# Kernel optimization log

Hardware: AMD Instinct MI355X
Metric: run time of the kernel (lower is better)

Reference implementation:

```python
import jax, jax.numpy as jnp
import numpy as np

N, E = 50000, 800000          # nodes, edges
IN, H, C = 256, 4, 64          # in_channels, heads, per-head out channels
HID, OUT = 64, 40              # lin1 hidden, num classes
NEG_SLOPE = 0.2                # PyG GATConv default


def setup_inputs() -> dict:
    key = jax.random.key(0)
    ks = jax.random.split(key, 10)
    s = 0.05
    return {
        "x": jax.random.normal(ks[0], (N, IN), jnp.float32),
        "edge_index": jax.random.randint(ks[1], (2, E), 0, N, dtype=jnp.int64),
        "W": jax.random.normal(ks[2], (IN, H * C), jnp.float32) * s,     # GATConv lin (no bias)
        "att_src": jax.random.normal(ks[3], (H, C), jnp.float32) * s,
        "att_dst": jax.random.normal(ks[4], (H, C), jnp.float32) * s,
        "bias_conv": jnp.zeros((H * C,), jnp.float32),
        "W1": jax.random.normal(ks[5], (H * C, HID), jnp.float32) * s,
        "b1": jnp.zeros((HID,), jnp.float32),
        "W2": jax.random.normal(ks[6], (HID, OUT), jnp.float32) * s,
        "b2": jnp.zeros((OUT,), jnp.float32),
    }


def reference(x, edge_index, W, att_src, att_dst, bias_conv, W1, b1, W2, b2):
    n = x.shape[0]
    # PyG GATConv default: add self-loops (also guarantees no empty segments)
    loop = jnp.arange(n, dtype=edge_index.dtype)
    src = jnp.concatenate([edge_index[0], loop])  # [E+N]
    dst = jnp.concatenate([edge_index[1], loop])

    h = (x @ W).reshape(n, H, C)                         # [N,H,C]
    a_src = jnp.einsum('nhc,hc->nh', h, att_src)         # [N,H]
    a_dst = jnp.einsum('nhc,hc->nh', h, att_dst)

    # per-edge attention logits + segment softmax over incoming edges of dst
    e = jax.nn.leaky_relu(a_src[src] + a_dst[dst], NEG_SLOPE)   # [E+N,H]
    m = jax.ops.segment_max(e, dst, num_segments=n)             # [N,H]
    ex = jnp.exp(e - m[dst])
    denom = jax.ops.segment_sum(ex, dst, num_segments=n)
    alpha = ex / denom[dst]                                     # [E+N,H]

    # weighted scatter-aggregate of source features
    msg = alpha[:, :, None] * h[src]                            # [E+N,H,C]
    out = jax.ops.segment_sum(msg, dst, num_segments=n)         # [N,H,C]
    out = out.reshape(n, H * C) + bias_conv

    out = jax.nn.relu(out)              # .relu() after conv1 (dropout off in eval)
    out = jax.nn.relu(out @ W1 + b1)    # lin1 + relu
    return out @ W2 + b2                # lin2
```

## Files before the change

### kernel.cpp

```cpp
#include <hip/hip_runtime.h>
#include <math.h>

#define HEADS 4
#define CH 64
#define HC 256
#define SLOPE 0.2f
#define SLOT 64

typedef __attribute__((ext_vector_type(8))) short bf16x8;
typedef __attribute__((ext_vector_type(8))) unsigned short u16x8;
typedef __attribute__((ext_vector_type(4))) float f32x4;

__device__ __forceinline__ float4 ld4(const float* p){ return *(const float4*)p; }
__device__ __forceinline__ void st4(float* p, float4 v){ *(float4*)p = v; }
__device__ __forceinline__ float lrelu(float x){ return x > 0.f ? x : SLOPE * x; }
__device__ __forceinline__ unsigned short f2bf(float f){
  union { float f; unsigned int u; } v; v.f = f;
  unsigned int r = v.u + 0x7fffu + ((v.u >> 16) & 1u);
  return (unsigned short)(r >> 16);
}
__device__ __forceinline__ float bflo(unsigned int u){
  union { unsigned int u; float f; } v; v.u = u << 16; return v.f;
}
__device__ __forceinline__ float bfhi(unsigned int u){
  union { unsigned int u; float f; } v; v.u = u & 0xffff0000u; return v.f;
}
__device__ __forceinline__ void split2(float v, unsigned short& h, unsigned short& l){
  unsigned int u = __float_as_uint(v);
  h = (unsigned short)(u >> 16);
  float hf = __uint_as_float(u & 0xffff0000u);
  l = (unsigned short)(__float_as_uint(v - hf) >> 16);
}
__device__ __forceinline__ void dma16(const unsigned short* g, unsigned short* l){
  __builtin_amdgcn_global_load_lds(
      (const __attribute__((address_space(1))) unsigned int*)g,
      (__attribute__((address_space(3))) unsigned int*)l, 16, 0, 0);
}

__global__ __launch_bounds__(256) void k_pre(
    const float* __restrict__ W, const float* __restrict__ W1, const float* __restrict__ W2,
    unsigned short* __restrict__ Bhi, unsigned short* __restrict__ Blo,
    unsigned short* __restrict__ W1h, unsigned short* __restrict__ W1l,
    unsigned short* __restrict__ W2h, unsigned short* __restrict__ W2l,
    int* __restrict__ cnt, int Nn) {
  int b = blockIdx.x, t = threadIdx.x;
  if (b < 256) {
    int nn = b;
    unsigned short h, l;
    split2(W[(size_t)t*256 + nn], h, l);
    Bhi[(size_t)nn*256 + t] = h; Blo[(size_t)nn*256 + t] = l;
  } else if (b < 320) {
    int nn = b - 256;
    unsigned short h, l;
    split2(W1[(size_t)t*64 + nn], h, l);
    W1h[(size_t)nn*256 + t] = h; W1l[(size_t)nn*256 + t] = l;
  } else if (b < 368) {
    if (t < 64) {
      int nn = b - 320;
      float v = (nn < 40) ? W2[(size_t)t*40 + nn] : 0.f;
      unsigned short h, l;
      split2(v, h, l);
      W2h[(size_t)nn*64 + t] = h; W2l[(size_t)nn*64 + t] = l;
    }
  } else {
    int i = (b - 368)*256 + t;
    if (i < Nn) cnt[i] = 0;
  }
}

__global__ __launch_bounds__(256, 4) void k_gemmfill(const float* __restrict__ x,
    const unsigned short* __restrict__ Bhi_t, const unsigned short* __restrict__ Blo_t,
    unsigned short* __restrict__ hbf,
    const float* __restrict__ att_src, const float* __restrict__ att_dst,
    float* __restrict__ a_srcO, float* __restrict__ a_dstO, int M, int nFill,
    const int* __restrict__ ei, int* __restrict__ cnt, int* __restrict__ csrf,
    int E, int EN) {
  __shared__ __align__(16) unsigned short L[4*4096];
  int t = threadIdx.x;
  int b = blockIdx.x;
  if (b < nFill) {
    int base = b*2048 + t;
    int s0=0,d0=0,s1=0,d1=0,s2=0,d2=0,s3=0,d3=0;
    int s4=0,d4=0,s5=0,d5=0,s6=0,d6=0,s7=0,d7=0;
    int e0=base, e1=base+256, e2=base+512, e3=base+768;
    int e4=base+1024, e5=base+1280, e6=base+1536, e7=base+1792;
    bool q0=e0<EN,q1=e1<EN,q2=e2<EN,q3=e3<EN,q4=e4<EN,q5=e5<EN,q6=e6<EN,q7=e7<EN;
    if (q0) { if (e0<E) { s0=ei[e0]; d0=ei[E+e0]; } else { s0=e0-E; d0=s0; } }
    if (q1) { if (e1<E) { s1=ei[e1]; d1=ei[E+e1]; } else { s1=e1-E; d1=s1; } }
    if (q2) { if (e2<E) { s2=ei[e2]; d2=ei[E+e2]; } else { s2=e2-E; d2=s2; } }
    if (q3) { if (e3<E) { s3=ei[e3]; d3=ei[E+e3]; } else { s3=e3-E; d3=s3; } }
    if (q4) { if (e4<E) { s4=ei[e4]; d4=ei[E+e4]; } else { s4=e4-E; d4=s4; } }
    if (q5) { if (e5<E) { s5=ei[e5]; d5=ei[E+e5]; } else { s5=e5-E; d5=s5; } }
    if (q6) { if (e6<E) { s6=ei[e6]; d6=ei[E+e6]; } else { s6=e6-E; d6=s6; } }
    if (q7) { if (e7<E) { s7=ei[e7]; d7=ei[E+e7]; } else { s7=e7-E; d7=s7; } }
    if (q0) { int p = atomicAdd(&cnt[d0], 1); csrf[(d0<<6) + p] = s0; }
    if (q1) { int p = atomicAdd(&cnt[d1], 1); csrf[(d1<<6) + p] = s1; }
    if (q2) { int p = atomicAdd(&cnt[d2], 1); csrf[(d2<<6) + p] = s2; }
    if (q3) { int p = atomicAdd(&cnt[d3], 1); csrf[(d3<<6) + p] = s3; }
    if (q4) { int p = atomicAdd(&cnt[d4], 1); csrf[(d4<<6) + p] = s4; }
    if (q5) { int p = atomicAdd(&cnt[d5], 1); csrf[(d5<<6) + p] = s5; }
    if (q6) { int p = atomicAdd(&cnt[d6], 1); csrf[(d6<<6) + p] = s6; }
    if (q7) { int p = atomicAdd(&cnt[d7], 1); csrf[(d7<<6) + p] = s7; }
    return;
  }
  int gb = b - nFill;
  int lane = t & 63, w = t >> 6;
  int wr = w >> 1, wc = w & 1;
  int ln15 = lane & 15, lq = lane >> 4;
  int row0 = (gb >> 1) * 128, col0 = (gb & 1) * 128;

  f32x4 acc[4][4];
  #pragma unroll
  for (int i=0;i<4;i++)
    #pragma unroll
    for (int j=0;j<4;j++) acc[i][j] = (f32x4){0.f,0.f,0.f,0.f};

  int sA = w*128 + lane;
  int sB = sA + 64;
  int RA = sA>>3, uA = (sA&7)^(RA&7), idxA = (RA<<1)|(uA&1), segA = uA>>1;
  int RB = sB>>3, uB = (sB&7)^(RB&7), idxB = (RB<<1)|(uB&1), segB = uB>>1;
  size_t gB_a = (size_t)(col0+idxA)*256 + segA*8;
  size_t gB_b = (size_t)(col0+idxB)*256 + segB*8;
  int l0 = (w*128)*8, l1 = (w*128+64)*8;

  int ar = t >> 1, akh = t & 1;
  int arow = row0 + ar;
  bool avalid = arow < M;
  const float* xp = &x[(size_t)arow*256 + akh*16];
  int aR = ar >> 1;
  int u0w = ((2*akh+0) << 1) | (ar & 1);
  int u1w = ((2*akh+1) << 1) | (ar & 1);
  int as0 = aR*8 + (u0w ^ (aR & 7));
  int as1 = aR*8 + (u1w ^ (aR & 7));

  for (int c = 0; c < 8; c++) {
    int k0 = c*32;
    dma16(Bhi_t + gB_a + k0, &L[2*4096 + l0]);
    dma16(Bhi_t + gB_b + k0, &L[2*4096 + l1]);
    dma16(Blo_t + gB_a + k0, &L[3*4096 + l0]);
    dma16(Blo_t + gB_b + k0, &L[3*4096 + l1]);
    float4 f0 = make_float4(0,0,0,0), f1 = f0, f2 = f0, f3 = f0;
    if (avalid) {
      const float* xc = xp + k0;
      f0 = ld4(xc); f1 = ld4(xc+4); f2 = ld4(xc+8); f3 = ld4(xc+12);
    }
    u16x8 h0, l0v, h1, l1v;
    unsigned short hh, ll;
    split2(f0.x,hh,ll); h0[0]=hh; l0v[0]=ll;
    split2(f0.y,hh,ll); h0[1]=hh; l0v[1]=ll;
    split2(f0.z,hh,ll); h0[2]=hh; l0v[2]=ll;
    split2(f0.w,hh,ll); h0[3]=hh; l0v[3]=ll;
    split2(f1.x,hh,ll); h0[4]=hh; l0v[4]=ll;
    split2(f1.y,hh,ll); h0[5]=hh; l0v[5]=ll;
    split2(f1.z,hh,ll); h0[6]=hh; l0v[6]=ll;
    split2(f1.w,hh,ll); h0[7]=hh; l0v[7]=ll;
    split2(f2.x,hh,ll); h1[0]=hh; l1v[0]=ll;
    split2(f2.y,hh,ll); h1[1]=hh; l1v[1]=ll;
    split2(f2.z,hh,ll); h1[2]=hh; l1v[2]=ll;
    split2(f2.w,hh,ll); h1[3]=hh; l1v[3]=ll;
    split2(f3.x,hh,ll); h1[4]=hh; l1v[4]=ll;
    split2(f3.y,hh,ll); h1[5]=hh; l1v[5]=ll;
    split2(f3.z,hh,ll); h1[6]=hh; l1v[6]=ll;
    split2(f3.w,hh,ll); h1[7]=hh; l1v[7]=ll;
    *(u16x8*)&L[0*4096 + as0*8] = h0;
    *(u16x8*)&L[1*4096 + as0*8] = l0v;
    *(u16x8*)&L[0*4096 + as1*8] = h1;
    *(u16x8*)&L[1*4096 + as1*8] = l1v;
    __syncthreads();

    bf16x8 bh[4], bl[4];
    #pragma unroll
    for (int j = 0; j < 4; j++) {
      int nn = wc*64 + j*16 + ln15;
      int R = nn >> 1, u = (lq << 1) | (nn & 1);
      int s = R*8 + (u ^ (R & 7));
      bh[j] = *(bf16x8*)&L[2*4096 + s*8];
      bl[j] = *(bf16x8*)&L[3*4096 + s*8];
    }
    #pragma unroll
    for (int i = 0; i < 4; i++) {
      int r = wr*64 + i*16 + ln15;
      int R = r >> 1, u = (lq << 1) | (r & 1);
      int s = R*8 + (u ^ (R & 7));
      bf16x8 ah = *(bf16x8*)&L[0*4096 + s*8];
      bf16x8 al = *(bf16x8*)&L[1*4096 + s*8];
      #pragma unroll
      for (int j = 0; j < 4; j++) {
        acc[i][j] = __builtin_amdgcn_mfma_f32_16x16x32_bf16(ah, bh[j], acc[i][j], 0,0,0);
        acc[i][j] = __builtin_amdgcn_mfma_f32_16x16x32_bf16(al, bh[j], acc[i][j], 0,0,0);
        acc[i][j] = __builtin_amdgcn_mfma_f32_16x16x32_bf16(ah, bl[j], acc[i][j], 0,0,0);
      }
    }
    __syncthreads();
  }
  unsigned short* hb2 = hbf + (size_t)(gb & 1) * M * 128;
  #pragma unroll
  for (int i = 0; i < 4; i++) {
    #pragma unroll
    for (int r = 0; r < 4; r++) {
      int row = row0 + wr*64 + i*16 + lq*4 + r;
      if (row < M) {
        #pragma unroll
        for (int j = 0; j < 4; j++) {
          int col = wc*64 + j*16 + ln15;
          hb2[(size_t)row*128 + col] = f2bf(acc[i][j][r]);
        }
      }
    }
  }
  int head = (gb & 1)*2 + wc;
  float asv[4], adv[4];
  #pragma unroll
  for (int j=0;j<4;j++){
    asv[j] = att_src[head*CH + j*16 + ln15];
    adv[j] = att_dst[head*CH + j*16 + ln15];
  }
  #pragma unroll
  for (int i = 0; i < 4; i++) {
    #pragma unroll
    for (int r = 0; r < 4; r++) {
      float ps = acc[i][0][r]*asv[0] + acc[i][1][r]*asv[1]
               + acc[i][2][r]*asv[2] + acc[i][3][r]*asv[3];
      float pd = acc[i][0][r]*adv[0] + acc[i][1][r]*adv[1]
               + acc[i][2][r]*adv[2] + acc[i][3][r]*adv[3];
      #pragma unroll
      for (int m=8; m>=1; m>>=1) { ps += __shfl_xor(ps, m); pd += __shfl_xor(pd, m); }
      if (ln15 == 0) {
        int row = row0 + wr*64 + i*16 + lq*4 + r;
        if (row < M) { a_srcO[row*4+head] = ps; a_dstO[row*4+head] = pd; }
      }
    }
  }
}

__global__ __launch_bounds__(256) void k_gat(const unsigned short* __restrict__ hbf,
    const float* __restrict__ a_src, const float* __restrict__ a_dst,
    const int* __restrict__ cnt, const int* __restrict__ csrf,
    const float* __restrict__ bias, unsigned short* __restrict__ outbf,
    int N, int nBlk) {
  int w = threadIdx.x >> 6, lane = threadIdx.x & 63;
  int q = lane >> 4, cl = lane & 15;
  int pass = (blockIdx.x >= nBlk) ? 1 : 0;
  int blk = blockIdx.x - pass*nBlk;
  int n = blk*16 + w*4 + q;
  int c0 = cl * 8;
  int hd = cl >> 3;
  int eb = q * 16;
  const unsigned short* hb = hbf + (size_t)pass * N * 128;
  const int* row = &csrf[(size_t)n << 6];

  __shared__ float s_p[4][64][2];

  float2 ad = *(const float2*)&a_dst[(size_t)n*4 + pass*2];
  float dsum = 0.f;
  float acc[8];
  #pragma unroll
  for (int k=0;k<8;k++) acc[k]=0.f;

  int deg = cnt[n];
  int dm = max(deg, __shfl_xor(deg, 16));
  dm = max(dm, __shfl_xor(dm, 32));

  for (int cb = 0; cb < dm; cb += 16) {
    int cnt16 = min(16, deg - cb);
    int cm  = min(16, dm - cb);
    int s = 0;
    float p0 = 0.f, p1 = 0.f;
    if (cl < cnt16) {
      s = row[cb + cl];
      float2 as = *(const float2*)&a_src[(size_t)s*4 + pass*2];
      p0 = __expf(lrelu(as.x + ad.x));
      p1 = __expf(lrelu(as.y + ad.y));
    }
    *(float2*)&s_p[w][eb + cl][0] = make_float2(p0, p1);

    bool v0 = 0 < cnt16, v1 = 1 < cnt16, v2 = 2 < cnt16, v3 = 3 < cnt16;
    uint4 u0 = make_uint4(0,0,0,0), u1 = u0, u2 = u0, u3 = u0;
    int ss;
    ss = __shfl(s, eb + 0); if (v0) u0 = *(const uint4*)&hb[(size_t)ss*128 + c0];
    ss = __shfl(s, eb + 1); if (v1) u1 = *(const uint4*)&hb[(size_t)ss*128 + c0];
    ss = __shfl(s, eb + 2); if (v2) u2 = *(const uint4*)&hb[(size_t)ss*128 + c0];
    ss = __shfl(s, eb + 3); if (v3) u3 = *(const uint4*)&hb[(size_t)ss*128 + c0];
    for (int g = 0; g < cm; g += 4) {
      int f0 = g+4, f1 = g+5, f2 = g+6, f3 = g+7;
      bool w0 = f0 < cnt16, w1 = f1 < cnt16, w2 = f2 < cnt16, w3 = f3 < cnt16;
      uint4 t0 = make_uint4(0,0,0,0), t1 = t0, t2 = t0, t3 = t0;
      ss = __shfl(s, eb + (f0 & 15)); if (w0) t0 = *(const uint4*)&hb[(size_t)ss*128 + c0];
      ss = __shfl(s, eb + (f1 & 15)); if (w1) t1 = *(const uint4*)&hb[(size_t)ss*128 + c0];
      ss = __shfl(s, eb + (f2 & 15)); if (w2) t2 = *(const uint4*)&hb[(size_t)ss*128 + c0];
      ss = __shfl(s, eb + (f3 & 15)); if (w3) t3 = *(const uint4*)&hb[(size_t)ss*128 + c0];
      if (v0) {
        float pw = s_p[w][eb + g    ][hd]; dsum += pw;
        acc[0] += pw*bflo(u0.x); acc[1] += pw*bfhi(u0.x);
        acc[2] += pw*bflo(u0.y); acc[3] += pw*bfhi(u0.y);
        acc[4] += pw*bflo(u0.z); acc[5] += pw*bfhi(u0.z);
        acc[6] += pw*bflo(u0.w); acc[7] += pw*bfhi(u0.w);
      }
      if (v1) {
        float pw = s_p[w][eb + g + 1][hd]; dsum += pw;
        acc[0] += pw*bflo(u1.x); acc[1] += pw*bfhi(u1.x);
        acc[2] += pw*bflo(u1.y); acc[3] += pw*bfhi(u1.y);
        acc[4] += pw*bflo(u1.z); acc[5] += pw*bfhi(u1.z);
        acc[6] += pw*bflo(u1.w); acc[7] += pw*bfhi(u1.w);
      }
      if (v2) {
        float pw = s_p[w][eb + g + 2][hd]; dsum += pw;
        acc[0] += pw*bflo(u2.x); acc[1] += pw*bfhi(u2.x);
        acc[2] += pw*bflo(u2.y); acc[3] += pw*bfhi(u2.y);
        acc[4] += pw*bflo(u2.z); acc[5] += pw*bfhi(u2.z);
        acc[6] += pw*bflo(u2.w); acc[7] += pw*bfhi(u2.w);
      }
      if (v3) {
        float pw = s_p[w][eb + g + 3][hd]; dsum += pw;
        acc[0] += pw*bflo(u3.x); acc[1] += pw*bfhi(u3.x);
        acc[2] += pw*bflo(u3.y); acc[3] += pw*bfhi(u3.y);
        acc[4] += pw*bflo(u3.z); acc[5] += pw*bfhi(u3.z);
        acc[6] += pw*bflo(u3.w); acc[7] += pw*bfhi(u3.w);
      }
      u0 = t0; u1 = t1; u2 = t2; u3 = t3;
      v0 = w0; v1 = w1; v2 = w2; v3 = w3;
    }
  }
  float inv = 1.f / dsum;
  float4 b0 = ld4(&bias[pass*128 + c0]);
  float4 b1 = ld4(&bias[pass*128 + c0 + 4]);
  uint4 o;
  o.x = (unsigned)f2bf(fmaxf(acc[0]*inv + b0.x, 0.f))
      | ((unsigned)f2bf(fmaxf(acc[1]*inv + b0.y, 0.f)) << 16);
  o.y = (unsigned)f2bf(fmaxf(acc[2]*inv + b0.z, 0.f))
      | ((unsigned)f2bf(fmaxf(acc[3]*inv + b0.w, 0.f)) << 16);
  o.z = (unsigned)f2bf(fmaxf(acc[4]*inv + b1.x, 0.f))
      | ((unsigned)f2bf(fmaxf(acc[5]*inv + b1.y, 0.f)) << 16);
  o.w = (unsigned)f2bf(fmaxf(acc[6]*inv + b1.z, 0.f))
      | ((unsigned)f2bf(fmaxf(acc[7]*inv + b1.w, 0.f)) << 16);
  *(uint4*)&outbf[(size_t)n*HC + pass*128 + c0] = o;
}

__global__ __launch_bounds__(256) void k_mlp(const unsigned short* __restrict__ Cbf,
    const unsigned short* __restrict__ W1h, const unsigned short* __restrict__ W1l,
    const unsigned short* __restrict__ W2h, const unsigned short* __restrict__ W2l,
    const float* __restrict__ b1, const float* __restrict__ b2,
    float* __restrict__ out, int M) {
  __shared__ __align__(16) unsigned short Abuf[2048];
  __shared__ __align__(16) unsigned short Hs[64*72];
  int t = threadIdx.x, lane = t & 63, w = t >> 6;
  int ln15 = lane & 15, lq = lane >> 4;
  int row0 = blockIdx.x * 64;

  f32x4 acc1[4];
  #pragma unroll
  for (int j=0;j<4;j++) acc1[j] = (f32x4){0.f,0.f,0.f,0.f};

  int sA = t;
  int rA = sA >> 2, segA = (sA & 3) ^ ((rA >> 1) & 3);
  size_t gA = (size_t)(row0 + rA) * 256 + segA*8;

  for (int c = 0; c < 8; c++) {
    int k0 = c*32;
    dma16(Cbf + gA + k0, &Abuf[sA*8]);
    __syncthreads();
    int r = w*16 + ln15;
    int s = r*4 + (lq ^ ((r >> 1) & 3));
    bf16x8 a = *(bf16x8*)&Abuf[s*8];
    #pragma unroll
    for (int j = 0; j < 4; j++) {
      int n = j*16 + ln15;
      int k = k0 + lq*8;
      bf16x8 bh = *(const bf16x8*)&W1h[(size_t)n*256 + k];
      bf16x8 bl = *(const bf16x8*)&W1l[(size_t)n*256 + k];
      acc1[j] = __builtin_amdgcn_mfma_f32_16x16x32_bf16(a, bh, acc1[j], 0,0,0);
      acc1[j] = __builtin_amdgcn_mfma_f32_16x16x32_bf16(a, bl, acc1[j], 0,0,0);
    }
    __syncthreads();
  }
  #pragma unroll
  for (int j = 0; j < 4; j++) {
    int col = j*16 + ln15;
    float bv = b1[col];
    #pragma unroll
    for (int r = 0; r < 4; r++) {
      int rl = w*16 + lq*4 + r;
      Hs[rl*72 + col] = f2bf(fmaxf(acc1[j][r] + bv, 0.f));
    }
  }
  f32x4 acc2[3];
  #pragma unroll
  for (int j=0;j<3;j++) acc2[j] = (f32x4){0.f,0.f,0.f,0.f};
  #pragma unroll
  for (int kf = 0; kf < 2; kf++) {
    int m = w*16 + ln15;
    bf16x8 a2 = *(bf16x8*)&Hs[m*72 + kf*32 + lq*8];
    #pragma unroll
    for (int j = 0; j < 3; j++) {
      int n = j*16 + ln15;
      int k = kf*32 + lq*8;
      bf16x8 wh = *(const bf16x8*)&W2h[(size_t)n*64 + k];
      bf16x8 wl = *(const bf16x8*)&W2l[(size_t)n*64 + k];
      acc2[j] = __builtin_amdgcn_mfma_f32_16x16x32_bf16(a2, wh, acc2[j], 0,0,0);
      acc2[j] = __builtin_amdgcn_mfma_f32_16x16x32_bf16(a2, wl, acc2[j], 0,0,0);
    }
  }
  #pragma unroll
  for (int j = 0; j < 3; j++) {
    int col = j*16 + ln15;
    if (col < 40) {
      float bv = b2[col];
      #pragma unroll
      for (int r = 0; r < 4; r++) {
        int row = row0 + w*16 + lq*4 + r;
        if (row < M) out[(size_t)row*40 + col] = acc2[j][r] + bv;
      }
    }
  }
}

extern "C" void kernel_launch(void* const* d_in, const int* in_sizes, int n_in,
                              void* d_out, int out_size, void* d_ws, size_t ws_size,
                              hipStream_t stream) {
  const int Nn = in_sizes[0] / HC;
  const int E  = in_sizes[1] / 2;
  const int Mpad = (Nn + 127) & ~127;
  const float* x        = (const float*)d_in[0];
  const int*   ei       = (const int*)d_in[1];
  const float* W        = (const float*)d_in[2];
  const float* att_src  = (const float*)d_in[3];
  const float* att_dst  = (const float*)d_in[4];
  const float* biasconv = (const float*)d_in[5];
  const float* W1       = (const float*)d_in[6];
  const float* b1       = (const float*)d_in[7];
  const float* W2       = (const float*)d_in[8];
  const float* b2       = (const float*)d_in[9];
  float* out = (float*)d_out;

  size_t off = 0;
  auto alloc = [&](size_t bytes)->void* {
    void* p = (void*)((char*)d_ws + off);
    off += (bytes + 255) & ~(size_t)255;
    return p;
  };
  unsigned short* hbf  = (unsigned short*)alloc((size_t)Nn*HC*sizeof(unsigned short));
  unsigned short* outc = (unsigned short*)alloc((size_t)Mpad*HC*sizeof(unsigned short));
  unsigned short* Bhi = (unsigned short*)alloc((size_t)256*256*sizeof(unsigned short));
  unsigned short* Blo = (unsigned short*)alloc((size_t)256*256*sizeof(unsigned short));
  unsigned short* W1h = (unsigned short*)alloc((size_t)64*256*sizeof(unsigned short));
  unsigned short* W1l = (unsigned short*)alloc((size_t)64*256*sizeof(unsigned short));
  unsigned short* W2h = (unsigned short*)alloc((size_t)48*64*sizeof(unsigned short));
  unsigned short* W2l = (unsigned short*)alloc((size_t)48*64*sizeof(unsigned short));
  float* a_src_v  = (float*)alloc((size_t)Nn*4*sizeof(float));
  float* a_dst_v  = (float*)alloc((size_t)Nn*4*sizeof(float));
  int*   cnt      = (int*)alloc((size_t)Nn*sizeof(int));
  int*   csrf     = (int*)alloc((size_t)Nn*SLOT*sizeof(int));
  (void)ws_size; (void)n_in; (void)out_size;

  dim3 blk(256);
  int nGemm = 2 * (Mpad/128);
  int EN = E + Nn;
  int nFill = (EN + 2047)/2048;
  int nZero = (Nn + 255)/256;
  int nBlkGat = Nn/16;

  k_pre<<<dim3(368 + nZero), blk, 0, stream>>>(W, W1, W2,
      Bhi, Blo, W1h, W1l, W2h, W2l, cnt, Nn);
  k_gemmfill<<<dim3(nFill + nGemm), blk, 0, stream>>>(x, Bhi, Blo, hbf,
      att_src, att_dst, a_src_v, a_dst_v, Nn, nFill, ei, cnt, csrf, E, EN);
  k_gat<<<dim3(2*nBlkGat), blk, 0, stream>>>(hbf, a_src_v, a_dst_v,
                                             cnt, csrf, biasconv, outc, Nn, nBlkGat);
  k_mlp<<<dim3(Mpad/64), blk, 0, stream>>>(outc, W1h, W1l, W2h, W2l, b1, b2, out, Nn);
}
```

Baseline: 268.0 us.

## Fuse GAT aggregation with MLP and store all heads in one feature row

The GAT aggregation and the two-layer MLP become a single kernel. Each block aggregates 8 nodes across all four heads, keeps the bf16 conv output in shared memory and runs lin1/lin2 with MFMA directly, so the intermediate [N,256] buffer is no longer written and reread. The projected features are now stored as a full 256-wide row per node instead of two 128-column halves, so one gather reads all heads. Counter zeroing moves to hipMemsetAsync. In exchange, the MLP MFMAs use only 8 of 16 rows, the grid assumes N is divisible by 8, and W1/W2 are re-fetched per small block.

New measurement: 270.6 us. Within noise of the previous version (+1.0%).

```diff
diff --git a/kernel.cpp b/kernel.cpp
--- a/kernel.cpp
+++ b/kernel.cpp
@@ -41,8 +41,7 @@
     const float* __restrict__ W, const float* __restrict__ W1, const float* __restrict__ W2,
     unsigned short* __restrict__ Bhi, unsigned short* __restrict__ Blo,
     unsigned short* __restrict__ W1h, unsigned short* __restrict__ W1l,
-    unsigned short* __restrict__ W2h, unsigned short* __restrict__ W2l,
-    int* __restrict__ cnt, int Nn) {
+    unsigned short* __restrict__ W2h, unsigned short* __restrict__ W2l) {
   int b = blockIdx.x, t = threadIdx.x;
   if (b < 256) {
     int nn = b;
@@ -54,7 +53,7 @@
     unsigned short h, l;
     split2(W1[(size_t)t*64 + nn], h, l);
     W1h[(size_t)nn*256 + t] = h; W1l[(size_t)nn*256 + t] = l;
-  } else if (b < 368) {
+  } else {
     if (t < 64) {
       int nn = b - 320;
       float v = (nn < 40) ? W2[(size_t)t*40 + nn] : 0.f;
@@ -62,9 +61,6 @@
       split2(v, h, l);
       W2h[(size_t)nn*64 + t] = h; W2l[(size_t)nn*64 + t] = l;
     }
-  } else {
-    int i = (b - 368)*256 + t;
-    if (i < Nn) cnt[i] = 0;
   }
 }
 
@@ -193,7 +189,6 @@
     }
     __syncthreads();
   }
-  unsigned short* hb2 = hbf + (size_t)(gb & 1) * M * 128;
   #pragma unroll
   for (int i = 0; i < 4; i++) {
     #pragma unroll
@@ -202,8 +197,8 @@
       if (row < M) {
         #pragma unroll
         for (int j = 0; j < 4; j++) {
-          int col = wc*64 + j*16 + ln15;
-          hb2[(size_t)row*128 + col] = f2bf(acc[i][j][r]);
+          int col = col0 + wc*64 + j*16 + ln15;
+          hbf[(size_t)row*HC + col] = f2bf(acc[i][j][r]);
         }
       }
     }
@@ -233,85 +228,90 @@
   }
 }
 
-__global__ __launch_bounds__(256) void k_gat(const unsigned short* __restrict__ hbf,
-    const float* __restrict__ a_src, const float* __restrict__ a_dst,
+__global__ __launch_bounds__(256) void k_gatmlp(const unsigned short* __restrict__ hbf,
+    const float4* __restrict__ a_src, const float4* __restrict__ a_dst,
     const int* __restrict__ cnt, const int* __restrict__ csrf,
-    const float* __restrict__ bias, unsigned short* __restrict__ outbf,
-    int N, int nBlk) {
-  int w = threadIdx.x >> 6, lane = threadIdx.x & 63;
-  int q = lane >> 4, cl = lane & 15;
-  int pass = (blockIdx.x >= nBlk) ? 1 : 0;
-  int blk = blockIdx.x - pass*nBlk;
-  int n = blk*16 + w*4 + q;
+    const float* __restrict__ bias,
+    const unsigned short* __restrict__ W1h, const unsigned short* __restrict__ W1l,
+    const unsigned short* __restrict__ W2h, const unsigned short* __restrict__ W2l,
+    const float* __restrict__ b1, const float* __restrict__ b2,
+    float* __restrict__ out) {
+  int t = threadIdx.x;
+  int w = t >> 6, lane = t & 63;
+  int half = lane >> 5, cl = lane & 31;
+  int nid = w*2 + half;
+  int n = blockIdx.x * 8 + nid;
   int c0 = cl * 8;
-  int hd = cl >> 3;
-  int eb = q * 16;
-  const unsigned short* hb = hbf + (size_t)pass * N * 128;
-  const int* row = &csrf[(size_t)n << 6];
-
-  __shared__ float s_p[4][64][2];
-
-  float2 ad = *(const float2*)&a_dst[(size_t)n*4 + pass*2];
+  int hd8 = cl >> 3;
+  int eb = half * 32;
+
+  __shared__ float s_p[4][64][4];
+  __shared__ __align__(16) unsigned short mlpA[8][264];
+  __shared__ __align__(16) unsigned short Hs[8][72];
+
+  float4 ad = a_dst[n];
   float dsum = 0.f;
   float acc[8];
   #pragma unroll
   for (int k=0;k<8;k++) acc[k]=0.f;
 
+  const int* row = &csrf[(size_t)n << 6];
   int deg = cnt[n];
-  int dm = max(deg, __shfl_xor(deg, 16));
-  dm = max(dm, __shfl_xor(dm, 32));
-
-  for (int cb = 0; cb < dm; cb += 16) {
-    int cnt16 = min(16, deg - cb);
-    int cm  = min(16, dm - cb);
+  int dm = max(deg, __shfl_xor(deg, 32));
+
+  for (int cb = 0; cb < dm; cb += 32) {
+    int cnt32 = min(32, deg - cb);
+    int cm  = min(32, dm - cb);
     int s = 0;
-    float p0 = 0.f, p1 = 0.f;
-    if (cl < cnt16) {
+    float4 p = make_float4(0.f,0.f,0.f,0.f);
+    if (cl < cnt32) {
       s = row[cb + cl];
-      float2 as = *(const float2*)&a_src[(size_t)s*4 + pass*2];
-      p0 = __expf(lrelu(as.x + ad.x));
-      p1 = __expf(lrelu(as.y + ad.y));
-    }
-    *(float2*)&s_p[w][eb + cl][0] = make_float2(p0, p1);
-
-    bool v0 = 0 < cnt16, v1 = 1 < cnt16, v2 = 2 < cnt16, v3 = 3 < cnt16;
+      float4 as = a_src[s];
+      p.x = __expf(lrelu(as.x + ad.x));
+      p.y = __expf(lrelu(as.y + ad.y));
+      p.z = __expf(lrelu(as.z + ad.z));
+      p.w = __expf(lrelu(as.w + ad.w));
+    }
+    st4(&s_p[w][eb + cl][0], p);
+
+    bool v0 = 0 < cnt32, v1 = 1 < cnt32, v2 = 2 < cnt32, v3 = 3 < cnt32;
     uint4 u0 = make_uint4(0,0,0,0), u1 = u0, u2 = u0, u3 = u0;
     int ss;
-    ss = __shfl(s, eb + 0); if (v0) u0 = *(const uint4*)&hb[(size_t)ss*128 + c0];
-    ss = __shfl(s, eb + 1); if (v1) u1 = *(const uint4*)&hb[(size_t)ss*128 + c0];
-    ss = __shfl(s, eb + 2); if (v2) u2 = *(const uint4*)&hb[(size_t)ss*128 + c0];
-    ss = __shfl(s, eb + 3); if (v3) u3 = *(const uint4*)&hb[(size_t)ss*128 + c0];
+    ss = __shfl(s, eb + 0); if (v0) u0 = *(const uint4*)&hbf[(size_t)ss*HC + c0];
+    ss = __shfl(s, eb + 1); if (v1) u1 = *(const uint4*)&hbf[(size_t)ss*HC + c0];
+    ss = __shfl(s, eb + 2); if (v2) u2 = *(const uint4*)&hbf[(size_t)ss*HC + c0];
+    ss = __shfl(s, eb + 3); if (v3) u3 = *(const uint4*)&hbf[(size_t)ss*HC + c0];
     for (int g = 0; g < cm; g += 4) {
       int f0 = g+4, f1 = g+5, f2 = g+6, f3 = g+7;
-      bool w0 = f0 < cnt16, w1 = f1 < cnt16, w2 = f2 < cnt16, w3 = f3 < cnt16;
+      bool w0 = f0 < cnt32, w1 = f1 < cnt32, w2 = f2 < cnt32, w3 = f3 < cnt32;
       uint4 t0 = make_uint4(0,0,0,0), t1 = t0, t2 = t0, t3 = t0;
-      ss = __shfl(s, eb + (f0 & 15)); if (w0) t0 = *(const uint4*)&hb[(size_t)ss*128 + c0];
-      ss = __shfl(s, eb + (f1 & 15)); if (w1) t1 = *(const uint4*)&hb[(size_t)ss*128 + c0];
-      ss = __shfl(s, eb + (f2 & 15)); if (w2) t2 = *(const uint4*)&hb[(size_t)ss*128 + c0];
-      ss = __shfl(s, eb + (f3 & 15)); if (w3) t3 = *(const uint4*)&hb[(size_t)ss*128 + c0];
+      ss = __shfl(s, eb + (f0 & 31)); if (w0) t0 = *(const uint4*)&hbf[(size_t)ss*HC + c0];
+      ss = __shfl(s, eb + (f1 & 31)); if (w1) t1 = *(const uint4*)&hbf[(size_t)ss*HC + c0];
+      ss = __shfl(s, eb + (f2 & 31)); if (w2) t2 = *(const uint4*)&hbf[(size_t)ss*HC + c0];
+      ss = __shfl(s, eb + (f3 & 31)); if (w3) t3 = *(const uint4*)&hbf[(size_t)ss*HC + c0];
       if (v0) {
-        float pw = s_p[w][eb + g    ][hd]; dsum += pw;
+        float pw = s_p[w][eb + g    ][hd8]; dsum += pw;
         acc[0] += pw*bflo(u0.x); acc[1] += pw*bfhi(u0.x);
         acc[2] += pw*bflo(u0.y); acc[3] += pw*bfhi(u0.y);
         acc[4] += pw*bflo(u0.z); acc[5] += pw*bfhi(u0.z);
         acc[6] += pw*bflo(u0.w); acc[7] += pw*bfhi(u0.w);
       }
       if (v1) {
-        float pw = s_p[w][eb + g + 1][hd]; dsum += pw;
+        float pw = s_p[w][eb + g + 1][hd8]; dsum += pw;
         acc[0] += pw*bflo(u1.x); acc[1] += pw*bfhi(u1.x);
         acc[2] += pw*bflo(u1.y); acc[3] += pw*bfhi(u1.y);
         acc[4] += pw*bflo(u1.z); acc[5] += pw*bfhi(u1.z);
         acc[6] += pw*bflo(u1.w); acc[7] += pw*bfhi(u1.w);
       }
       if (v2) {
-        float pw = s_p[w][eb + g + 2][hd]; dsum += pw;
+        float pw = s_p[w][eb + g + 2][hd8]; dsum += pw;
         acc[0] += pw*bflo(u2.x); acc[1] += pw*bfhi(u2.x);
         acc[2] += pw*bflo(u2.y); acc[3] += pw*bfhi(u2.y);
         acc[4] += pw*bflo(u2.z); acc[5] += pw*bfhi(u2.z);
         acc[6] += pw*bflo(u2.w); acc[7] += pw*bfhi(u2.w);
       }
       if (v3) {
-        float pw = s_p[w][eb + g + 3][hd]; dsum += pw;
+        float pw = s_p[w][eb + g + 3][hd8]; dsum += pw;
         acc[0] += pw*bflo(u3.x); acc[1] += pw*bfhi(u3.x);
         acc[2] += pw*bflo(u3.y); acc[3] += pw*bfhi(u3.y);
         acc[4] += pw*bflo(u3.z); acc[5] += pw*bfhi(u3.z);
@@ -322,93 +322,60 @@
     }
   }
   float inv = 1.f / dsum;
-  float4 b0 = ld4(&bias[pass*128 + c0]);
-  float4 b1 = ld4(&bias[pass*128 + c0 + 4]);
+  float4 bv0 = ld4(&bias[c0]);
+  float4 bv1 = ld4(&bias[c0 + 4]);
   uint4 o;
-  o.x = (unsigned)f2bf(fmaxf(acc[0]*inv + b0.x, 0.f))
-      | ((unsigned)f2bf(fmaxf(acc[1]*inv + b0.y, 0.f)) << 16);
-  o.y = (unsigned)f2bf(fmaxf(acc[2]*inv + b0.z, 0.f))
-      | ((unsigned)f2bf(fmaxf(acc[3]*inv + b0.w, 0.f)) << 16);
-  o.z = (unsigned)f2bf(fmaxf(acc[4]*inv + b1.x, 0.f))
-      | ((unsigned)f2bf(fmaxf(acc[5]*inv + b1.y, 0.f)) << 16);
-  o.w = (unsigned)f2bf(fmaxf(acc[6]*inv + b1.z, 0.f))
-      | ((unsigned)f2bf(fmaxf(acc[7]*inv + b1.w, 0.f)) << 16);
-  *(uint4*)&outbf[(size_t)n*HC + pass*128 + c0] = o;
-}
-
-__global__ __launch_bounds__(256) void k_mlp(const unsigned short* __restrict__ Cbf,
-    const unsigned short* __restrict__ W1h, const unsigned short* __restrict__ W1l,
-    const unsigned short* __restrict__ W2h, const unsigned short* __restrict__ W2l,
-    const float* __restrict__ b1, const float* __restrict__ b2,
-    float* __restrict__ out, int M) {
-  __shared__ __align__(16) unsigned short Abuf[2048];
-  __shared__ __align__(16) unsigned short Hs[64*72];
-  int t = threadIdx.x, lane = t & 63, w = t >> 6;
+  o.x = (unsigned)f2bf(fmaxf(acc[0]*inv + bv0.x, 0.f))
+      | ((unsigned)f2bf(fmaxf(acc[1]*inv + bv0.y, 0.f)) << 16);
+  o.y = (unsigned)f2bf(fmaxf(acc[2]*inv + bv0.z, 0.f))
+      | ((unsigned)f2bf(fmaxf(acc[3]*inv + bv0.w, 0.f)) << 16);
+  o.z = (unsigned)f2bf(fmaxf(acc[4]*inv + bv1.x, 0.f))
+      | ((unsigned)f2bf(fmaxf(acc[5]*inv + bv1.y, 0.f)) << 16);
+  o.w = (unsigned)f2bf(fmaxf(acc[6]*inv + bv1.z, 0.f))
+      | ((unsigned)f2bf(fmaxf(acc[7]*inv + bv1.w, 0.f)) << 16);
+  *(uint4*)&mlpA[nid][c0] = o;
+  __syncthreads();
+
   int ln15 = lane & 15, lq = lane >> 4;
-  int row0 = blockIdx.x * 64;
-
-  f32x4 acc1[4];
-  #pragma unroll
-  for (int j=0;j<4;j++) acc1[j] = (f32x4){0.f,0.f,0.f,0.f};
-
-  int sA = t;
-  int rA = sA >> 2, segA = (sA & 3) ^ ((rA >> 1) & 3);
-  size_t gA = (size_t)(row0 + rA) * 256 + segA*8;
-
-  for (int c = 0; c < 8; c++) {
-    int k0 = c*32;
-    dma16(Cbf + gA + k0, &Abuf[sA*8]);
-    __syncthreads();
-    int r = w*16 + ln15;
-    int s = r*4 + (lq ^ ((r >> 1) & 3));
-    bf16x8 a = *(bf16x8*)&Abuf[s*8];
-    #pragma unroll
-    for (int j = 0; j < 4; j++) {
-      int n = j*16 + ln15;
-      int k = k0 + lq*8;
-      bf16x8 bh = *(const bf16x8*)&W1h[(size_t)n*256 + k];
-      bf16x8 bl = *(const bf16x8*)&W1l[(size_t)n*256 + k];
-      acc1[j] = __builtin_amdgcn_mfma_f32_16x16x32_bf16(a, bh, acc1[j], 0,0,0);
-      acc1[j] = __builtin_amdgcn_mfma_f32_16x16x32_bf16(a, bl, acc1[j], 0,0,0);
-    }
-    __syncthreads();
-  }
-  #pragma unroll
-  for (int j = 0; j < 4; j++) {
-    int col = j*16 + ln15;
-    float bv = b1[col];
-    #pragma unroll
-    for (int r = 0; r < 4; r++) {
-      int rl = w*16 + lq*4 + r;
-      Hs[rl*72 + col] = f2bf(fmaxf(acc1[j][r] + bv, 0.f));
-    }
-  }
-  f32x4 acc2[3];
-  #pragma unroll
-  for (int j=0;j<3;j++) acc2[j] = (f32x4){0.f,0.f,0.f,0.f};
-  #pragma unroll
-  for (int kf = 0; kf < 2; kf++) {
-    int m = w*16 + ln15;
-    bf16x8 a2 = *(bf16x8*)&Hs[m*72 + kf*32 + lq*8];
-    #pragma unroll
-    for (int j = 0; j < 3; j++) {
-      int n = j*16 + ln15;
+  int ncol = w*16 + ln15;
+  f32x4 acc1 = (f32x4){0.f,0.f,0.f,0.f};
+  #pragma unroll
+  for (int kf = 0; kf < 8; kf++) {
+    int k = kf*32 + lq*8;
+    bf16x8 a = (ln15 < 8) ? *(const bf16x8*)&mlpA[ln15][k]
+                          : (bf16x8){0,0,0,0,0,0,0,0};
+    bf16x8 bh = *(const bf16x8*)&W1h[(size_t)ncol*256 + k];
+    bf16x8 bl = *(const bf16x8*)&W1l[(size_t)ncol*256 + k];
+    acc1 = __builtin_amdgcn_mfma_f32_16x16x32_bf16(a, bh, acc1, 0,0,0);
+    acc1 = __builtin_amdgcn_mfma_f32_16x16x32_bf16(a, bl, acc1, 0,0,0);
+  }
+  float b1v = b1[ncol];
+  #pragma unroll
+  for (int r = 0; r < 4; r++) {
+    int rr = lq*4 + r;
+    if (rr < 8) Hs[rr][ncol] = f2bf(fmaxf(acc1[r] + b1v, 0.f));
+  }
+  __syncthreads();
+
+  if (w < 3) {
+    int col = w*16 + ln15;
+    f32x4 acc2 = (f32x4){0.f,0.f,0.f,0.f};
+    #pragma unroll
+    for (int kf = 0; kf < 2; kf++) {
       int k = kf*32 + lq*8;
-      bf16x8 wh = *(const bf16x8*)&W2h[(size_t)n*64 + k];
-      bf16x8 wl = *(const bf16x8*)&W2l[(size_t)n*64 + k];
-      acc2[j] = __builtin_amdgcn_mfma_f32_16x16x32_bf16(a2, wh, acc2[j], 0,0,0);
-      acc2[j] = __builtin_amdgcn_mfma_f32_16x16x32_bf16(a2, wl, acc2[j], 0,0,0);
-    }
-  }
-  #pragma unroll
-  for (int j = 0; j < 3; j++) {
-    int col = j*16 + ln15;
+      bf16x8 a2 = (ln15 < 8) ? *(const bf16x8*)&Hs[ln15][k]
+                             : (bf16x8){0,0,0,0,0,0,0,0};
+      bf16x8 wh = *(const bf16x8*)&W2h[(size_t)col*64 + k];
+      bf16x8 wl = *(const bf16x8*)&W2l[(size_t)col*64 + k];
+      acc2 = __builtin_amdgcn_mfma_f32_16x16x32_bf16(a2, wh, acc2, 0,0,0);
+      acc2 = __builtin_amdgcn_mfma_f32_16x16x32_bf16(a2, wl, acc2, 0,0,0);
+    }
     if (col < 40) {
-      float bv = b2[col];
+      float b2v = b2[col];
       #pragma unroll
       for (int r = 0; r < 4; r++) {
-        int row = row0 + w*16 + lq*4 + r;
-        if (row < M) out[(size_t)row*40 + col] = acc2[j][r] + bv;
+        int rr = lq*4 + r;
+        if (rr < 8) out[(size_t)(blockIdx.x*8 + rr)*40 + col] = acc2[r] + b2v;
       }
     }
   }
@@ -438,8 +405,7 @@
     off += (bytes + 255) & ~(size_t)255;
     return p;
   };
-  unsigned short* hbf  = (unsigned short*)alloc((size_t)Nn*HC*sizeof(unsigned short));
-  unsigned short* outc = (unsigned short*)alloc((size_t)Mpad*HC*sizeof(unsigned short));
+  unsigned short* hbf = (unsigned short*)alloc((size_t)Nn*HC*sizeof(unsigned short));
   unsigned short* Bhi = (unsigned short*)alloc((size_t)256*256*sizeof(unsigned short));
   unsigned short* Blo = (unsigned short*)alloc((size_t)256*256*sizeof(unsigned short));
   unsigned short* W1h = (unsigned short*)alloc((size_t)64*256*sizeof(unsigned short));
@@ -456,14 +422,13 @@
   int nGemm = 2 * (Mpad/128);
   int EN = E + Nn;
   int nFill = (EN + 2047)/2048;
-  int nZero = (Nn + 255)/256;
-  int nBlkGat = Nn/16;
-
-  k_pre<<<dim3(368 + nZero), blk, 0, stream>>>(W, W1, W2,
-      Bhi, Blo, W1h, W1l, W2h, W2l, cnt, Nn);
+
+  hipMemsetAsync(cnt, 0, (size_t)Nn*sizeof(int), stream);
+  k_pre<<<dim3(368), blk, 0, stream>>>(W, W1, W2,
+      Bhi, Blo, W1h, W1l, W2h, W2l);
   k_gemmfill<<<dim3(nFill + nGemm), blk, 0, stream>>>(x, Bhi, Blo, hbf,
       att_src, att_dst, a_src_v, a_dst_v, Nn, nFill, ei, cnt, csrf, E, EN);
-  k_gat<<<dim3(2*nBlkGat), blk, 0, stream>>>(hbf, a_src_v, a_dst_v,
-                                             cnt, csrf, biasconv, outc, Nn, nBlkGat);
-  k_mlp<<<dim3(Mpad/64), blk, 0, stream>>>(outc, W1h, W1l, W2h, W2l, b1, b2, out, Nn);
-}
+  k_gatmlp<<<dim3(Nn/8), blk, 0, stream>>>(hbf, (const float4*)a_src_v,
+      (const float4*)a_dst_v, cnt, csrf, biasconv,
+      W1h, W1l, W2h, W2l, b1, b2, out);
+}
```

## Split GAT aggregation in halves and overlap MLP of first half with second

Applied to the files above, without the earlier changes.

The node range is split at a 128-aligned midpoint. The first half's GAT aggregation runs alone. Then one combined kernel runs the MLP for the first half alongside GAT for the second half, and a final kernel does the remaining MLP rows. The cnt zeroing moves from k_pre to hipMemsetAsync. The aim is to fill the GPU better and hide the MLP cost behind the gather-bound GAT work, at the cost of an extra launch and a larger shared-memory footprint in the combined kernel, which may lower occupancy.

Result: no change. 266.9 us (-0.4%).

```diff
diff --git a/kernel.cpp b/kernel.cpp
--- a/kernel.cpp
+++ b/kernel.cpp
@@ -41,8 +41,7 @@
     const float* __restrict__ W, const float* __restrict__ W1, const float* __restrict__ W2,
     unsigned short* __restrict__ Bhi, unsigned short* __restrict__ Blo,
     unsigned short* __restrict__ W1h, unsigned short* __restrict__ W1l,
-    unsigned short* __restrict__ W2h, unsigned short* __restrict__ W2l,
-    int* __restrict__ cnt, int Nn) {
+    unsigned short* __restrict__ W2h, unsigned short* __restrict__ W2l) {
   int b = blockIdx.x, t = threadIdx.x;
   if (b < 256) {
     int nn = b;
@@ -54,7 +53,7 @@
     unsigned short h, l;
     split2(W1[(size_t)t*64 + nn], h, l);
     W1h[(size_t)nn*256 + t] = h; W1l[(size_t)nn*256 + t] = l;
-  } else if (b < 368) {
+  } else {
     if (t < 64) {
       int nn = b - 320;
       float v = (nn < 40) ? W2[(size_t)t*40 + nn] : 0.f;
@@ -62,9 +61,6 @@
       split2(v, h, l);
       W2h[(size_t)nn*64 + t] = h; W2l[(size_t)nn*64 + t] = l;
     }
-  } else {
-    int i = (b - 368)*256 + t;
-    if (i < Nn) cnt[i] = 0;
   }
 }
 
@@ -233,23 +229,21 @@
   }
 }
 
-__global__ __launch_bounds__(256) void k_gat(const unsigned short* __restrict__ hbf,
+__device__ __forceinline__ void gat_body(const unsigned short* __restrict__ hbf,
     const float* __restrict__ a_src, const float* __restrict__ a_dst,
     const int* __restrict__ cnt, const int* __restrict__ csrf,
     const float* __restrict__ bias, unsigned short* __restrict__ outbf,
-    int N, int nBlk) {
-  int w = threadIdx.x >> 6, lane = threadIdx.x & 63;
+    int N, int n0, int nBlk, int bid, int t, float (*s_p)[64][2]) {
+  int w = t >> 6, lane = t & 63;
   int q = lane >> 4, cl = lane & 15;
-  int pass = (blockIdx.x >= nBlk) ? 1 : 0;
-  int blk = blockIdx.x - pass*nBlk;
-  int n = blk*16 + w*4 + q;
+  int pass = (bid >= nBlk) ? 1 : 0;
+  int blk = bid - pass*nBlk;
+  int n = n0 + blk*16 + w*4 + q;
   int c0 = cl * 8;
   int hd = cl >> 3;
   int eb = q * 16;
   const unsigned short* hb = hbf + (size_t)pass * N * 128;
   const int* row = &csrf[(size_t)n << 6];
-
-  __shared__ float s_p[4][64][2];
 
   float2 ad = *(const float2*)&a_dst[(size_t)n*4 + pass*2];
   float dsum = 0.f;
@@ -336,16 +330,14 @@
   *(uint4*)&outbf[(size_t)n*HC + pass*128 + c0] = o;
 }
 
-__global__ __launch_bounds__(256) void k_mlp(const unsigned short* __restrict__ Cbf,
+__device__ __forceinline__ void mlp64_body(const unsigned short* __restrict__ Cbf,
     const unsigned short* __restrict__ W1h, const unsigned short* __restrict__ W1l,
     const unsigned short* __restrict__ W2h, const unsigned short* __restrict__ W2l,
     const float* __restrict__ b1, const float* __restrict__ b2,
-    float* __restrict__ out, int M) {
-  __shared__ __align__(16) unsigned short Abuf[2048];
-  __shared__ __align__(16) unsigned short Hs[64*72];
-  int t = threadIdx.x, lane = t & 63, w = t >> 6;
+    float* __restrict__ out, int M, int row0, int t,
+    unsigned short* Abuf, unsigned short* Hs) {
+  int lane = t & 63, w = t >> 6;
   int ln15 = lane & 15, lq = lane >> 4;
-  int row0 = blockIdx.x * 64;
 
   f32x4 acc1[4];
   #pragma unroll
@@ -412,6 +404,47 @@
       }
     }
   }
+}
+
+__global__ __launch_bounds__(256) void k_gat(const unsigned short* __restrict__ hbf,
+    const float* __restrict__ a_src, const float* __restrict__ a_dst,
+    const int* __restrict__ cnt, const int* __restrict__ csrf,
+    const float* __restrict__ bias, unsigned short* __restrict__ outbf,
+    int N, int n0, int nBlk) {
+  __shared__ float s_p[4][64][2];
+  gat_body(hbf, a_src, a_dst, cnt, csrf, bias, outbf, N, n0, nBlk,
+           blockIdx.x, threadIdx.x, s_p);
+}
+
+__global__ __launch_bounds__(256) void k_gatmlp2(const unsigned short* __restrict__ hbf,
+    const float* __restrict__ a_src, const float* __restrict__ a_dst,
+    const int* __restrict__ cnt, const int* __restrict__ csrf,
+    const float* __restrict__ bias, unsigned short* __restrict__ outc,
+    const unsigned short* __restrict__ W1h, const unsigned short* __restrict__ W1l,
+    const unsigned short* __restrict__ W2h, const unsigned short* __restrict__ W2l,
+    const float* __restrict__ b1, const float* __restrict__ b2,
+    float* __restrict__ out, int N, int split, int nBlk2, int nMlp) {
+  __shared__ __align__(16) unsigned short Abuf[2048];
+  __shared__ __align__(16) unsigned short Hs[64*72];
+  __shared__ float s_p[4][64][2];
+  int b = blockIdx.x, t = threadIdx.x;
+  if (b < nMlp) {
+    mlp64_body(outc, W1h, W1l, W2h, W2l, b1, b2, out, N, b*64, t, Abuf, Hs);
+    return;
+  }
+  gat_body(hbf, a_src, a_dst, cnt, csrf, bias, outc, N, split, nBlk2,
+           b - nMlp, t, s_p);
+}
+
+__global__ __launch_bounds__(256) void k_mlp64(const unsigned short* __restrict__ Cbf,
+    const unsigned short* __restrict__ W1h, const unsigned short* __restrict__ W1l,
+    const unsigned short* __restrict__ W2h, const unsigned short* __restrict__ W2l,
+    const float* __restrict__ b1, const float* __restrict__ b2,
+    float* __restrict__ out, int M, int r0) {
+  __shared__ __align__(16) unsigned short Abuf[2048];
+  __shared__ __align__(16) unsigned short Hs[64*72];
+  mlp64_body(Cbf, W1h, W1l, W2h, W2l, b1, b2, out, M,
+             r0 + blockIdx.x*64, threadIdx.x, Abuf, Hs);
 }
 
 extern "C" void kernel_launch(void* const* d_in, const int* in_sizes, int n_in,
@@ -456,14 +489,24 @@
   int nGemm = 2 * (Mpad/128);
   int EN = E + Nn;
   int nFill = (EN + 2047)/2048;
-  int nZero = (Nn + 255)/256;
-  int nBlkGat = Nn/16;
-
-  k_pre<<<dim3(368 + nZero), blk, 0, stream>>>(W, W1, W2,
-      Bhi, Blo, W1h, W1l, W2h, W2l, cnt, Nn);
+
+  int split = ((Nn/2)/128)*128;
+  int n2 = Nn - split;
+  int nBlk1 = split/16;
+  int nBlk2 = n2/16;
+  int nMlp1 = split/64;
+  int nMlp2 = (n2 + 63)/64;
+
+  hipMemsetAsync(cnt, 0, (size_t)Nn*sizeof(int), stream);
+  k_pre<<<dim3(368), blk, 0, stream>>>(W, W1, W2,
+      Bhi, Blo, W1h, W1l, W2h, W2l);
   k_gemmfill<<<dim3(nFill + nGemm), blk, 0, stream>>>(x, Bhi, Blo, hbf,
       att_src, att_dst, a_src_v, a_dst_v, Nn, nFill, ei, cnt, csrf, E, EN);
-  k_gat<<<dim3(2*nBlkGat), blk, 0, stream>>>(hbf, a_src_v, a_dst_v,
-                                             cnt, csrf, biasconv, outc, Nn, nBlkGat);
-  k_mlp<<<dim3(Mpad/64), blk, 0, stream>>>(outc, W1h, W1l, W2h, W2l, b1, b2, out, Nn);
-}
+  k_gat<<<dim3(2*nBlk1), blk, 0, stream>>>(hbf, a_src_v, a_dst_v,
+      cnt, csrf, biasconv, outc, Nn, 0, nBlk1);
+  k_gatmlp2<<<dim3(nMlp1 + 2*nBlk2), blk, 0, stream>>>(hbf, a_src_v, a_dst_v,
+      cnt, csrf, biasconv, outc, W1h, W1l, W2h, W2l, b1, b2, out,
+      Nn, split, nBlk2, nMlp1);
+  k_mlp64<<<dim3(nMlp2), blk, 0, stream>>>(outc, W1h, W1l, W2h, W2l,
+      b1, b2, out, Nn, split);
+}
```
